# Kernel tuning notes

Measured on AMD Instinct MI355X. Metric: run time of the kernel, lower is better.

The kernel has to match this reference:

```python
import jax, jax.numpy as jnp
import numpy as np

NUM_HEADS = 16
HEAD_DIM = 64
WINDOW = 512
D_MODEL = NUM_HEADS * HEAD_DIM
BATCH = 2
SEQ = 2048


def setup_inputs() -> dict:
    key = jax.random.key(0)
    k1, k2, k3 = jax.random.split(key, 3)
    x = jax.random.normal(k1, (BATCH, SEQ, D_MODEL), dtype=jnp.float32)
    # Dense layer params (lecun_normal-like scale for stability)
    qkv_kernel = jax.random.normal(k2, (D_MODEL, 3 * NUM_HEADS * HEAD_DIM), dtype=jnp.float32) / np.sqrt(D_MODEL)
    qkv_bias = jnp.zeros((3 * NUM_HEADS * HEAD_DIM,), dtype=jnp.float32)
    out_kernel = jax.random.normal(k3, (NUM_HEADS * HEAD_DIM, D_MODEL), dtype=jnp.float32) / np.sqrt(D_MODEL)
    out_bias = jnp.zeros((D_MODEL,), dtype=jnp.float32)
    return {"x": x, "qkv_kernel": qkv_kernel, "qkv_bias": qkv_bias,
            "out_kernel": out_kernel, "out_bias": out_bias}


def reference(x, qkv_kernel, qkv_bias, out_kernel, out_bias):
    b, s, d = x.shape
    qkv = x @ qkv_kernel + qkv_bias                       # (b, s, 3*H*hd)
    qkv = qkv.reshape(b, s, 3, NUM_HEADS, HEAD_DIM)
    q = qkv[:, :, 0].transpose(0, 2, 1, 3)                # (b, H, s, hd)
    k = qkv[:, :, 1].transpose(0, 2, 1, 3)
    v = qkv[:, :, 2].transpose(0, 2, 1, 3)
    scale = 1.0 / jnp.sqrt(jnp.float32(HEAD_DIM)).astype(x.dtype)
    scores = jnp.einsum('bhqd,bhkd->bhqk', q, k) * scale  # (b, H, s, s)
    rows = jnp.arange(s)[:, None]
    cols = jnp.arange(s)[None, :]
    window_mask = (rows - cols >= 0) & (rows - cols < WINDOW)
    scores = jnp.where(window_mask[None, None], scores, jnp.asarray(-1e9, scores.dtype))
    attn = jax.nn.softmax(scores, axis=-1)
    out = jnp.einsum('bhqk,bhkd->bhqd', attn, v)          # (b, H, s, hd)
    out = out.transpose(0, 2, 1, 3).reshape(b, s, -1)
    return out @ out_kernel + out_bias
```

## Files before the change

### kernel.cpp

```cpp
#include <hip/hip_runtime.h>
#include <cstdint>
#include <cstddef>

#define NUM_HEADS 16
#define HEAD_DIM  64
#define WINDOW    512
#define D_MODEL   1024
#define BATCH     2
#define SEQ       2048
#define MTOT      (BATCH*SEQ)
#define NQKV      (3*D_MODEL)

typedef short bf16x8 __attribute__((ext_vector_type(8)));
typedef float f32x4  __attribute__((ext_vector_type(4)));

__device__ __forceinline__ f32x4 mfma16(bf16x8 a, bf16x8 b, f32x4 c) {
  return __builtin_amdgcn_mfma_f32_16x16x32_bf16(a, b, c, 0, 0, 0);
}

__device__ __forceinline__ unsigned short f2bf(float f) {
  unsigned int u = __float_as_uint(f);
  u += 0x7fffu + ((u >> 16) & 1u);
  return (unsigned short)(u >> 16);
}
__device__ __forceinline__ float bf2f(unsigned short b) {
  return __uint_as_float(((unsigned int)b) << 16);
}

__device__ __forceinline__ void gld16(const unsigned short* g, unsigned short* l) {
  __builtin_amdgcn_global_load_lds(
      (const __attribute__((address_space(1))) unsigned int*)g,
      (__attribute__((address_space(3))) unsigned int*)l, 16, 0, 0);
}

__global__ __launch_bounds__(256) void cvt_bf16_kernel(const float* __restrict__ in,
                                                       unsigned short* __restrict__ out) {
  int i = (blockIdx.x * 256 + threadIdx.x) * 4;
  float4 v = *(const float4*)(in + i);
  ushort4 o;
  o.x = f2bf(v.x); o.y = f2bf(v.y); o.z = f2bf(v.z); o.w = f2bf(v.w);
  *(ushort4*)(out + i) = o;
}

__global__ __launch_bounds__(256) void transpose_cvt_kernel(const float* __restrict__ in,
                                                            unsigned short* __restrict__ out,
                                                            int R, int C) {
  __shared__ float tile[32][33];
  int tx = threadIdx.x, ty = threadIdx.y;
  int c0 = blockIdx.x * 32, r0 = blockIdx.y * 32;
#pragma unroll
  for (int i = 0; i < 32; i += 8)
    tile[ty + i][tx] = in[(size_t)(r0 + ty + i) * C + c0 + tx];
  __syncthreads();
#pragma unroll
  for (int i = 0; i < 32; i += 8)
    out[(size_t)(c0 + ty + i) * R + r0 + tx] = f2bf(tile[tx][ty + i]);
}

template<bool SWAP>
__device__ __forceinline__ void gemm_mainloop(const unsigned short* __restrict__ A,
                                              const unsigned short* __restrict__ Bt,
                                              int K, int m0, int n0,
                                              unsigned short* sA, unsigned short* sB,
                                              f32x4 (&acc)[4][4]) {
  const int t = threadIdx.x;
  const int lane = t & 63, wave = t >> 6;
  const int wm = wave >> 1, wn = wave & 1;
  const int lhi = lane >> 4, llo = lane & 15;
  f32x4 zero = {0.f, 0.f, 0.f, 0.f};
#pragma unroll
  for (int i = 0; i < 4; ++i)
#pragma unroll
    for (int j = 0; j < 4; ++j) acc[i][j] = zero;

  const int cswz = (((t & 3) ^ ((t >> 3) & 3)) << 3);
  const unsigned short* gA = A  + (size_t)(m0 + (t >> 2)) * K + cswz;
  const unsigned short* gB = Bt + (size_t)(n0 + (t >> 2)) * K + cswz;
  const size_t rowskip = (size_t)64 * K;
  unsigned short* lA = sA + t * 8;
  unsigned short* lB = sB + t * 8;
  const int rsw = (lhi ^ ((llo >> 1) & 3)) * 8;
  const unsigned short* rA = sA + (wm * 64 + llo) * 32 + rsw;
  const unsigned short* rB = sB + (wn * 64 + llo) * 32 + rsw;

  for (int k0 = 0; k0 < K; k0 += 32) {
    gld16(gA, lA); gld16(gA + rowskip, lA + 2048);
    gld16(gB, lB); gld16(gB + rowskip, lB + 2048);
    gA += 32; gB += 32;
    __syncthreads();
    bf16x8 af[4], bfr[4];
#pragma unroll
    for (int i = 0; i < 4; ++i) af[i]  = *(const bf16x8*)(rA + i * 512);
#pragma unroll
    for (int i = 0; i < 4; ++i) bfr[i] = *(const bf16x8*)(rB + i * 512);
#pragma unroll
    for (int i = 0; i < 4; ++i)
#pragma unroll
      for (int j = 0; j < 4; ++j)
        acc[i][j] = SWAP ? mfma16(bfr[j], af[i], acc[i][j])
                         : mfma16(af[i], bfr[j], acc[i][j]);
    __syncthreads();
  }
}

__global__ __launch_bounds__(256) void qkv_gemm_kernel(const unsigned short* __restrict__ Xb,
                                                       const unsigned short* __restrict__ Wt,
                                                       const float* __restrict__ bias,
                                                       unsigned short* __restrict__ Qw,
                                                       unsigned short* __restrict__ Kw,
                                                       unsigned short* __restrict__ Vtw) {
  __shared__ __align__(16) unsigned short sA[128 * 32];
  __shared__ __align__(16) unsigned short sB[128 * 32];
  f32x4 acc[4][4];
  const int m0 = blockIdx.y * 128, n0 = blockIdx.x * 128;
  const int t = threadIdx.x, lane = t & 63, wave = t >> 6;
  const int wm = wave >> 1, wn = wave & 1, lhi = lane >> 4, llo = lane & 15;

  if (n0 < 2048) {
    gemm_mainloop<false>(Xb, Wt, D_MODEL, m0, n0, sA, sB, acc);
#pragma unroll
    for (int ti = 0; ti < 4; ++ti) {
#pragma unroll
      for (int tj = 0; tj < 4; ++tj) {
        int n = n0 + wn * 64 + tj * 16 + llo;
        float bv = bias[n];
        int c = n >> 10, h = (n >> 6) & 15, d = n & 63;
#pragma unroll
        for (int r = 0; r < 4; ++r) {
          int m = m0 + wm * 64 + ti * 16 + lhi * 4 + r;
          int b = m >> 11, s = m & 2047;
          int bh = b * 16 + h;
          float v = acc[ti][tj][r] + bv;
          size_t idx = ((size_t)(bh * 2048 + s)) * 64 + d;
          if (c == 0) Qw[idx] = f2bf(v * 0.125f);
          else        Kw[idx] = f2bf(v);
        }
      }
    }
  } else {
    gemm_mainloop<true>(Xb, Wt, D_MODEL, m0, n0, sA, sB, acc);
#pragma unroll
    for (int ti = 0; ti < 4; ++ti) {
      int m = m0 + wm * 64 + ti * 16 + llo;
      int b = m >> 11, s = m & 2047;
#pragma unroll
      for (int tj = 0; tj < 4; ++tj) {
        int nb = n0 + wn * 64 + tj * 16 + lhi * 4;
        float4 bv = *(const float4*)(bias + nb);
        int h = (nb >> 6) & 15, dbase = nb & 63;
        int bh = b * 16 + h;
        float bvr[4] = {bv.x, bv.y, bv.z, bv.w};
#pragma unroll
        for (int r = 0; r < 4; ++r)
          Vtw[(size_t)(bh * 64 + dbase + r) * 2048 + s] = f2bf(acc[ti][tj][r] + bvr[r]);
      }
    }
  }
}

__global__ __launch_bounds__(256) void attn_kernel(const unsigned short* __restrict__ Qw,
                                                   const unsigned short* __restrict__ Kw,
                                                   const unsigned short* __restrict__ Vtw,
                                                   unsigned short* __restrict__ AO) {
  __shared__ __align__(16) unsigned short sK[2][64 * 64];
  __shared__ __align__(16) unsigned short sV[2][64 * 64];
  __shared__ __align__(16) unsigned short sP[4][16 * 72];
  const int t = threadIdx.x, lane = t & 63, wave = t >> 6;
  const int lhi = lane >> 4, llo = lane & 15;
  const int bh = blockIdx.x;
  const int q0 = (15 - blockIdx.y) << 7;
  const unsigned short* Qb = Qw  + (size_t)bh * 2048 * 64;
  const unsigned short* Kb = Kw  + (size_t)bh * 2048 * 64;
  const unsigned short* Vb = Vtw + (size_t)bh * 64 * 2048;

  const int qrow0 = q0 + wave * 16 + llo;
  bf16x8 qf[2][2];
  qf[0][0] = *(const bf16x8*)(Qb + (size_t)qrow0 * 64 + lhi * 8);
  qf[0][1] = *(const bf16x8*)(Qb + (size_t)qrow0 * 64 + 32 + lhi * 8);
  qf[1][0] = *(const bf16x8*)(Qb + (size_t)(qrow0 + 64) * 64 + lhi * 8);
  qf[1][1] = *(const bf16x8*)(Qb + (size_t)(qrow0 + 64) * 64 + 32 + lhi * 8);

  const int srow = t >> 3;
  const int scol = ((t & 7) ^ (srow & 7)) * 8;
  const int cpos  = (lhi ^ (llo & 7)) * 8;
  const int cposx = cpos ^ 32;

  float m_i[2] = {-1e30f, -1e30f}, l_i[2] = {0.f, 0.f};
  f32x4 o[2][4];
  f32x4 zero = {0.f, 0.f, 0.f, 0.f};
#pragma unroll
  for (int qs = 0; qs < 2; ++qs)
#pragma unroll
    for (int td = 0; td < 4; ++td) o[qs][td] = zero;

  const int kt_lo = (q0 > 511) ? ((q0 - 511) >> 6) : 0;
  const int kt_hi = (q0 + 64) >> 6;

  {
    const int k0 = kt_lo << 6;
    unsigned short* dK = sK[kt_lo & 1];
    unsigned short* dV = sV[kt_lo & 1];
    gld16(Kb + (size_t)(k0 + srow) * 64 + scol,      dK + t * 8);
    gld16(Kb + (size_t)(k0 + srow + 32) * 64 + scol, dK + t * 8 + 2048);
    gld16(Vb + (size_t)srow * 2048 + k0 + scol,        dV + t * 8);
    gld16(Vb + (size_t)(srow + 32) * 2048 + k0 + scol, dV + t * 8 + 2048);
  }

  for (int kt = kt_lo; kt <= kt_hi; ++kt) {
    __syncthreads();
    if (kt < kt_hi) {
      const int k0n = (kt + 1) << 6;
      unsigned short* dK = sK[(kt + 1) & 1];
      unsigned short* dV = sV[(kt + 1) & 1];
      gld16(Kb + (size_t)(k0n + srow) * 64 + scol,      dK + t * 8);
      gld16(Kb + (size_t)(k0n + srow + 32) * 64 + scol, dK + t * 8 + 2048);
      gld16(Vb + (size_t)srow * 2048 + k0n + scol,        dV + t * 8);
      gld16(Vb + (size_t)(srow + 32) * 2048 + k0n + scol, dV + t * 8 + 2048);
    }
    const unsigned short* bK = sK[kt & 1];
    const unsigned short* bV = sV[kt & 1];
    const int k0 = kt << 6;

#pragma unroll
    for (int qs = 0; qs < 2; ++qs) {
      const int qmin = q0 + qs * 64;
      if (k0 > qmin + 63 || k0 + 63 < qmin - (WINDOW - 1)) continue;
      const int qrow = qrow0 + qs * 64;

      f32x4 st[4];
#pragma unroll
      for (int tk = 0; tk < 4; ++tk) {
        const unsigned short* kr = bK + (tk * 16 + llo) * 64;
        bf16x8 kf0 = *(const bf16x8*)(kr + cpos);
        bf16x8 kf1 = *(const bf16x8*)(kr + cposx);
        f32x4 z = zero;
        z = mfma16(kf0, qf[qs][0], z);
        z = mfma16(kf1, qf[qs][1], z);
        st[tk] = z;
      }

      const int kb = k0 + lhi * 4;
      float mx = -1e30f;
#pragma unroll
      for (int tk = 0; tk < 4; ++tk)
#pragma unroll
        for (int r = 0; r < 4; ++r) {
          int key = kb + tk * 16 + r;
          bool ok = (key <= qrow) && (qrow - key < WINDOW);
          float s = ok ? st[tk][r] : -1e30f;
          st[tk][r] = s;
          mx = fmaxf(mx, s);
        }
      mx = fmaxf(mx, __shfl_xor(mx, 16));
      mx = fmaxf(mx, __shfl_xor(mx, 32));
      float mn = fmaxf(m_i[qs], mx);
      float a  = __expf(m_i[qs] - mn);
      float rs = 0.f;
      unsigned short* pw = &sP[wave][llo * 72];
#pragma unroll
      for (int tk = 0; tk < 4; ++tk) {
        ushort4 pb;
        pb.x = f2bf(__expf(st[tk][0] - mn));
        pb.y = f2bf(__expf(st[tk][1] - mn));
        pb.z = f2bf(__expf(st[tk][2] - mn));
        pb.w = f2bf(__expf(st[tk][3] - mn));
        *(ushort4*)(pw + tk * 16 + lhi * 4) = pb;
        rs += bf2f(pb.x) + bf2f(pb.y) + bf2f(pb.z) + bf2f(pb.w);
      }
      rs += __shfl_xor(rs, 16);
      rs += __shfl_xor(rs, 32);
      l_i[qs] = l_i[qs] * a + rs;
      m_i[qs] = mn;

      float aR[4];
#pragma unroll
      for (int r = 0; r < 4; ++r) aR[r] = __shfl(a, lhi * 4 + r);
#pragma unroll
      for (int td = 0; td < 4; ++td)
#pragma unroll
        for (int r = 0; r < 4; ++r) o[qs][td][r] *= aR[r];

      bf16x8 pf0 = *(const bf16x8*)(pw + lhi * 8);
      bf16x8 pf1 = *(const bf16x8*)(pw + 32 + lhi * 8);
#pragma unroll
      for (int td = 0; td < 4; ++td) {
        const unsigned short* vr = bV + (td * 16 + llo) * 64;
        bf16x8 vf0 = *(const bf16x8*)(vr + cpos);
        bf16x8 vf1 = *(const bf16x8*)(vr + cposx);
        o[qs][td] = mfma16(pf0, vf0, o[qs][td]);
        o[qs][td] = mfma16(pf1, vf1, o[qs][td]);
      }
    }
  }

  const int b = bh >> 4, h = bh & 15;
#pragma unroll
  for (int qs = 0; qs < 2; ++qs) {
    float lR[4];
#pragma unroll
    for (int r = 0; r < 4; ++r) lR[r] = 1.f / __shfl(l_i[qs], lhi * 4 + r);
#pragma unroll
    for (int td = 0; td < 4; ++td)
#pragma unroll
      for (int r = 0; r < 4; ++r) {
        int qr = q0 + qs * 64 + wave * 16 + lhi * 4 + r;
        AO[(size_t)(b * 2048 + qr) * 1024 + h * 64 + td * 16 + llo] = f2bf(o[qs][td][r] * lR[r]);
      }
  }
}

__global__ __launch_bounds__(256) void out_gemm_kernel(const unsigned short* __restrict__ AO,
                                                       const unsigned short* __restrict__ Wt,
                                                       const float* __restrict__ bias,
                                                       float* __restrict__ out) {
  __shared__ __align__(16) unsigned short sA[128 * 32];
  __shared__ __align__(16) unsigned short sB[128 * 32];
  f32x4 acc[4][4];
  const int m0 = blockIdx.y * 128, n0 = blockIdx.x * 128;
  gemm_mainloop<false>(AO, Wt, D_MODEL, m0, n0, sA, sB, acc);

  const int t = threadIdx.x, lane = t & 63, wave = t >> 6;
  const int wm = wave >> 1, wn = wave & 1, lhi = lane >> 4, llo = lane & 15;
#pragma unroll
  for (int ti = 0; ti < 4; ++ti)
#pragma unroll
    for (int tj = 0; tj < 4; ++tj) {
      int n = n0 + wn * 64 + tj * 16 + llo;
      float bv = bias[n];
#pragma unroll
      for (int r = 0; r < 4; ++r) {
        int m = m0 + wm * 64 + ti * 16 + lhi * 4 + r;
        out[(size_t)m * D_MODEL + n] = acc[ti][tj][r] + bv;
      }
    }
}

extern "C" void kernel_launch(void* const* d_in, const int* in_sizes, int n_in,
                              void* d_out, int out_size, void* d_ws, size_t ws_size,
                              hipStream_t stream) {
  const float* x      = (const float*)d_in[0];
  const float* qkv_w  = (const float*)d_in[1];
  const float* qkv_b  = (const float*)d_in[2];
  const float* out_w  = (const float*)d_in[3];
  const float* out_b  = (const float*)d_in[4];
  float* out = (float*)d_out;
  char* ws = (char*)d_ws;

  unsigned short* Xb  = (unsigned short*)(ws);
  unsigned short* Wq  = (unsigned short*)(ws + ((size_t)8  << 20));
  unsigned short* Wo  = (unsigned short*)(ws + ((size_t)14 << 20));
  unsigned short* Qw  = (unsigned short*)(ws + ((size_t)16 << 20));
  unsigned short* Kw  = (unsigned short*)(ws + ((size_t)24 << 20));
  unsigned short* Vtw = (unsigned short*)(ws + ((size_t)32 << 20));
  unsigned short* AO  = (unsigned short*)(ws + ((size_t)40 << 20));

  cvt_bf16_kernel<<<MTOT * D_MODEL / 1024, 256, 0, stream>>>(x, Xb);
  transpose_cvt_kernel<<<dim3(NQKV / 32, D_MODEL / 32), dim3(32, 8), 0, stream>>>(qkv_w, Wq, D_MODEL, NQKV);
  transpose_cvt_kernel<<<dim3(D_MODEL / 32, D_MODEL / 32), dim3(32, 8), 0, stream>>>(out_w, Wo, D_MODEL, D_MODEL);
  qkv_gemm_kernel<<<dim3(NQKV / 128, MTOT / 128), 256, 0, stream>>>(Xb, Wq, qkv_b, Qw, Kw, Vtw);
  attn_kernel<<<dim3(BATCH * NUM_HEADS, SEQ / 128), 256, 0, stream>>>(Qw, Kw, Vtw, AO);
  out_gemm_kernel<<<dim3(D_MODEL / 128, MTOT / 128), 256, 0, stream>>>(AO, Wo, out_b, out);
}
```

Before: 190.7 us.

## Fuse prep kernels, double-buffer GEMM LDS, shrink attention and out-GEMM tiles

Merges the input conversion and both weight transposes into one prep launch. Double-buffers the GEMM shared-memory tiles so the next K slice loads while the current one computes, and drops one barrier per iteration. Attention blocks now cover 64 query rows instead of 128, and the output GEMM uses 64-row tiles; both double the block count for better occupancy at the cost of reloading more K/V and weight tiles. Doubling the LDS footprint may lower the number of resident blocks per CU.

```diff
diff --git a/kernel.cpp b/kernel.cpp
--- a/kernel.cpp
+++ b/kernel.cpp
@@ -33,21 +33,27 @@
       (__attribute__((address_space(3))) unsigned int*)l, 16, 0, 0);
 }
 
-__global__ __launch_bounds__(256) void cvt_bf16_kernel(const float* __restrict__ in,
-                                                       unsigned short* __restrict__ out) {
-  int i = (blockIdx.x * 256 + threadIdx.x) * 4;
-  float4 v = *(const float4*)(in + i);
-  ushort4 o;
-  o.x = f2bf(v.x); o.y = f2bf(v.y); o.z = f2bf(v.z); o.w = f2bf(v.w);
-  *(ushort4*)(out + i) = o;
-}
-
-__global__ __launch_bounds__(256) void transpose_cvt_kernel(const float* __restrict__ in,
-                                                            unsigned short* __restrict__ out,
-                                                            int R, int C) {
+__global__ __launch_bounds__(256) void prep_kernel(const float* __restrict__ x,
+                                                   const float* __restrict__ qkv_w,
+                                                   const float* __restrict__ out_w,
+                                                   unsigned short* __restrict__ Xb,
+                                                   unsigned short* __restrict__ Wq,
+                                                   unsigned short* __restrict__ Wo) {
   __shared__ float tile[32][33];
-  int tx = threadIdx.x, ty = threadIdx.y;
-  int c0 = blockIdx.x * 32, r0 = blockIdx.y * 32;
+  const int bid = blockIdx.x, t = threadIdx.x;
+  if (bid < 4096) {
+    int i = (bid * 256 + t) * 4;
+    float4 v = *(const float4*)(x + i);
+    ushort4 o;
+    o.x = f2bf(v.x); o.y = f2bf(v.y); o.z = f2bf(v.z); o.w = f2bf(v.w);
+    *(ushort4*)(Xb + i) = o;
+    return;
+  }
+  const float* in; unsigned short* out; int R, C, bx, by;
+  if (bid < 7168) { int b2 = bid - 4096; in = qkv_w; out = Wq; R = D_MODEL; C = NQKV; bx = b2 % 96; by = b2 / 96; }
+  else            { int b2 = bid - 7168; in = out_w; out = Wo; R = D_MODEL; C = D_MODEL; bx = b2 & 31; by = b2 >> 5; }
+  int tx = t & 31, ty = t >> 5;
+  int c0 = bx * 32, r0 = by * 32;
 #pragma unroll
   for (int i = 0; i < 32; i += 8)
     tile[ty + i][tx] = in[(size_t)(r0 + ty + i) * C + c0 + tx];
@@ -57,19 +63,20 @@
     out[(size_t)(c0 + ty + i) * R + r0 + tx] = f2bf(tile[tx][ty + i]);
 }
 
-template<bool SWAP>
-__device__ __forceinline__ void gemm_mainloop(const unsigned short* __restrict__ A,
-                                              const unsigned short* __restrict__ Bt,
-                                              int K, int m0, int n0,
-                                              unsigned short* sA, unsigned short* sB,
-                                              f32x4 (&acc)[4][4]) {
+template<int TI, bool SWAP>
+__device__ __forceinline__ void gemm_mainloop_db(const unsigned short* __restrict__ A,
+                                                 const unsigned short* __restrict__ Bt,
+                                                 int K, int m0, int n0,
+                                                 unsigned short* sA0, unsigned short* sA1,
+                                                 unsigned short* sB0, unsigned short* sB1,
+                                                 f32x4 (&acc)[TI][4]) {
   const int t = threadIdx.x;
   const int lane = t & 63, wave = t >> 6;
   const int wm = wave >> 1, wn = wave & 1;
   const int lhi = lane >> 4, llo = lane & 15;
   f32x4 zero = {0.f, 0.f, 0.f, 0.f};
 #pragma unroll
-  for (int i = 0; i < 4; ++i)
+  for (int i = 0; i < TI; ++i)
 #pragma unroll
     for (int j = 0; j < 4; ++j) acc[i][j] = zero;
 
@@ -77,29 +84,41 @@
   const unsigned short* gA = A  + (size_t)(m0 + (t >> 2)) * K + cswz;
   const unsigned short* gB = Bt + (size_t)(n0 + (t >> 2)) * K + cswz;
   const size_t rowskip = (size_t)64 * K;
-  unsigned short* lA = sA + t * 8;
-  unsigned short* lB = sB + t * 8;
-  const int rsw = (lhi ^ ((llo >> 1) & 3)) * 8;
-  const unsigned short* rA = sA + (wm * 64 + llo) * 32 + rsw;
-  const unsigned short* rB = sB + (wn * 64 + llo) * 32 + rsw;
-
-  for (int k0 = 0; k0 < K; k0 += 32) {
-    gld16(gA, lA); gld16(gA + rowskip, lA + 2048);
-    gld16(gB, lB); gld16(gB + rowskip, lB + 2048);
-    gA += 32; gB += 32;
+  const int ldsT = t * 8;
+  const int rsw  = (lhi ^ ((llo >> 1) & 3)) * 8;
+  const int aoff = (wm * (TI * 16) + llo) * 32 + rsw;
+  const int boff = (wn * 64 + llo) * 32 + rsw;
+
+  gld16(gA, sA0 + ldsT);
+  if (TI == 4) gld16(gA + rowskip, sA0 + ldsT + 2048);
+  gld16(gB, sB0 + ldsT);
+  gld16(gB + rowskip, sB0 + ldsT + 2048);
+
+  const int nIter = K >> 5;
+  for (int it = 0; it < nIter; ++it) {
     __syncthreads();
-    bf16x8 af[4], bfr[4];
-#pragma unroll
-    for (int i = 0; i < 4; ++i) af[i]  = *(const bf16x8*)(rA + i * 512);
-#pragma unroll
-    for (int i = 0; i < 4; ++i) bfr[i] = *(const bf16x8*)(rB + i * 512);
-#pragma unroll
-    for (int i = 0; i < 4; ++i)
+    unsigned short* cA = (it & 1) ? sA1 : sA0;
+    unsigned short* cB = (it & 1) ? sB1 : sB0;
+    if (it + 1 < nIter) {
+      unsigned short* nA = (it & 1) ? sA0 : sA1;
+      unsigned short* nB = (it & 1) ? sB0 : sB1;
+      gA += 32; gB += 32;
+      gld16(gA, nA + ldsT);
+      if (TI == 4) gld16(gA + rowskip, nA + ldsT + 2048);
+      gld16(gB, nB + ldsT);
+      gld16(gB + rowskip, nB + ldsT + 2048);
+    }
+    bf16x8 af[TI], bfr[4];
+#pragma unroll
+    for (int i = 0; i < TI; ++i) af[i]  = *(const bf16x8*)(cA + aoff + i * 512);
+#pragma unroll
+    for (int j = 0; j < 4; ++j)  bfr[j] = *(const bf16x8*)(cB + boff + j * 512);
+#pragma unroll
+    for (int i = 0; i < TI; ++i)
 #pragma unroll
       for (int j = 0; j < 4; ++j)
         acc[i][j] = SWAP ? mfma16(bfr[j], af[i], acc[i][j])
                          : mfma16(af[i], bfr[j], acc[i][j]);
-    __syncthreads();
   }
 }
 
@@ -109,15 +128,15 @@
                                                        unsigned short* __restrict__ Qw,
                                                        unsigned short* __restrict__ Kw,
                                                        unsigned short* __restrict__ Vtw) {
-  __shared__ __align__(16) unsigned short sA[128 * 32];
-  __shared__ __align__(16) unsigned short sB[128 * 32];
+  __shared__ __align__(16) unsigned short sA[2][128 * 32];
+  __shared__ __align__(16) unsigned short sB[2][128 * 32];
   f32x4 acc[4][4];
   const int m0 = blockIdx.y * 128, n0 = blockIdx.x * 128;
   const int t = threadIdx.x, lane = t & 63, wave = t >> 6;
   const int wm = wave >> 1, wn = wave & 1, lhi = lane >> 4, llo = lane & 15;
 
   if (n0 < 2048) {
-    gemm_mainloop<false>(Xb, Wt, D_MODEL, m0, n0, sA, sB, acc);
+    gemm_mainloop_db<4, false>(Xb, Wt, D_MODEL, m0, n0, sA[0], sA[1], sB[0], sB[1], acc);
 #pragma unroll
     for (int ti = 0; ti < 4; ++ti) {
 #pragma unroll
@@ -138,7 +157,7 @@
       }
     }
   } else {
-    gemm_mainloop<true>(Xb, Wt, D_MODEL, m0, n0, sA, sB, acc);
+    gemm_mainloop_db<4, true>(Xb, Wt, D_MODEL, m0, n0, sA[0], sA[1], sB[0], sB[1], acc);
 #pragma unroll
     for (int ti = 0; ti < 4; ++ti) {
       int m = m0 + wm * 64 + ti * 16 + llo;
@@ -168,33 +187,28 @@
   const int t = threadIdx.x, lane = t & 63, wave = t >> 6;
   const int lhi = lane >> 4, llo = lane & 15;
   const int bh = blockIdx.x;
-  const int q0 = (15 - blockIdx.y) << 7;
+  const int q0 = (31 - blockIdx.y) << 6;
   const unsigned short* Qb = Qw  + (size_t)bh * 2048 * 64;
   const unsigned short* Kb = Kw  + (size_t)bh * 2048 * 64;
   const unsigned short* Vb = Vtw + (size_t)bh * 64 * 2048;
 
-  const int qrow0 = q0 + wave * 16 + llo;
-  bf16x8 qf[2][2];
-  qf[0][0] = *(const bf16x8*)(Qb + (size_t)qrow0 * 64 + lhi * 8);
-  qf[0][1] = *(const bf16x8*)(Qb + (size_t)qrow0 * 64 + 32 + lhi * 8);
-  qf[1][0] = *(const bf16x8*)(Qb + (size_t)(qrow0 + 64) * 64 + lhi * 8);
-  qf[1][1] = *(const bf16x8*)(Qb + (size_t)(qrow0 + 64) * 64 + 32 + lhi * 8);
+  const int qrow = q0 + wave * 16 + llo;
+  bf16x8 qf0 = *(const bf16x8*)(Qb + (size_t)qrow * 64 + lhi * 8);
+  bf16x8 qf1 = *(const bf16x8*)(Qb + (size_t)qrow * 64 + 32 + lhi * 8);
 
   const int srow = t >> 3;
   const int scol = ((t & 7) ^ (srow & 7)) * 8;
   const int cpos  = (lhi ^ (llo & 7)) * 8;
   const int cposx = cpos ^ 32;
 
-  float m_i[2] = {-1e30f, -1e30f}, l_i[2] = {0.f, 0.f};
-  f32x4 o[2][4];
+  float m_i = -1e30f, l_i = 0.f;
+  f32x4 o[4];
   f32x4 zero = {0.f, 0.f, 0.f, 0.f};
 #pragma unroll
-  for (int qs = 0; qs < 2; ++qs)
-#pragma unroll
-    for (int td = 0; td < 4; ++td) o[qs][td] = zero;
+  for (int td = 0; td < 4; ++td) o[td] = zero;
 
   const int kt_lo = (q0 > 511) ? ((q0 - 511) >> 6) : 0;
-  const int kt_hi = (q0 + 64) >> 6;
+  const int kt_hi = q0 >> 6;
 
   {
     const int k0 = kt_lo << 6;
@@ -221,115 +235,105 @@
     const unsigned short* bV = sV[kt & 1];
     const int k0 = kt << 6;
 
-#pragma unroll
-    for (int qs = 0; qs < 2; ++qs) {
-      const int qmin = q0 + qs * 64;
-      if (k0 > qmin + 63 || k0 + 63 < qmin - (WINDOW - 1)) continue;
-      const int qrow = qrow0 + qs * 64;
-
-      f32x4 st[4];
-#pragma unroll
-      for (int tk = 0; tk < 4; ++tk) {
-        const unsigned short* kr = bK + (tk * 16 + llo) * 64;
-        bf16x8 kf0 = *(const bf16x8*)(kr + cpos);
-        bf16x8 kf1 = *(const bf16x8*)(kr + cposx);
-        f32x4 z = zero;
-        z = mfma16(kf0, qf[qs][0], z);
-        z = mfma16(kf1, qf[qs][1], z);
-        st[tk] = z;
+    f32x4 st[4];
+#pragma unroll
+    for (int tk = 0; tk < 4; ++tk) {
+      const unsigned short* kr = bK + (tk * 16 + llo) * 64;
+      bf16x8 kf0 = *(const bf16x8*)(kr + cpos);
+      bf16x8 kf1 = *(const bf16x8*)(kr + cposx);
+      f32x4 z = zero;
+      z = mfma16(kf0, qf0, z);
+      z = mfma16(kf1, qf1, z);
+      st[tk] = z;
+    }
+
+    const int kb = k0 + lhi * 4;
+    float mx = -1e30f;
+#pragma unroll
+    for (int tk = 0; tk < 4; ++tk)
+#pragma unroll
+      for (int r = 0; r < 4; ++r) {
+        int key = kb + tk * 16 + r;
+        bool ok = (key <= qrow) && (qrow - key < WINDOW);
+        float s = ok ? st[tk][r] : -1e30f;
+        st[tk][r] = s;
+        mx = fmaxf(mx, s);
       }
-
-      const int kb = k0 + lhi * 4;
-      float mx = -1e30f;
-#pragma unroll
-      for (int tk = 0; tk < 4; ++tk)
-#pragma unroll
-        for (int r = 0; r < 4; ++r) {
-          int key = kb + tk * 16 + r;
-          bool ok = (key <= qrow) && (qrow - key < WINDOW);
-          float s = ok ? st[tk][r] : -1e30f;
-          st[tk][r] = s;
-          mx = fmaxf(mx, s);
-        }
-      mx = fmaxf(mx, __shfl_xor(mx, 16));
-      mx = fmaxf(mx, __shfl_xor(mx, 32));
-      float mn = fmaxf(m_i[qs], mx);
-      float a  = __expf(m_i[qs] - mn);
-      float rs = 0.f;
-      unsigned short* pw = &sP[wave][llo * 72];
-#pragma unroll
-      for (int tk = 0; tk < 4; ++tk) {
-        ushort4 pb;
-        pb.x = f2bf(__expf(st[tk][0] - mn));
-        pb.y = f2bf(__expf(st[tk][1] - mn));
-        pb.z = f2bf(__expf(st[tk][2] - mn));
-        pb.w = f2bf(__expf(st[tk][3] - mn));
-        *(ushort4*)(pw + tk * 16 + lhi * 4) = pb;
-        rs += bf2f(pb.x) + bf2f(pb.y) + bf2f(pb.z) + bf2f(pb.w);
-      }
-      rs += __shfl_xor(rs, 16);
-      rs += __shfl_xor(rs, 32);
-      l_i[qs] = l_i[qs] * a + rs;
-      m_i[qs] = mn;
-
-      float aR[4];
-#pragma unroll
-      for (int r = 0; r < 4; ++r) aR[r] = __shfl(a, lhi * 4 + r);
-#pragma unroll
-      for (int td = 0; td < 4; ++td)
-#pragma unroll
-        for (int r = 0; r < 4; ++r) o[qs][td][r] *= aR[r];
-
-      bf16x8 pf0 = *(const bf16x8*)(pw + lhi * 8);
-      bf16x8 pf1 = *(const bf16x8*)(pw + 32 + lhi * 8);
-#pragma unroll
-      for (int td = 0; td < 4; ++td) {
-        const unsigned short* vr = bV + (td * 16 + llo) * 64;
-        bf16x8 vf0 = *(const bf16x8*)(vr + cpos);
-        bf16x8 vf1 = *(const bf16x8*)(vr + cposx);
-        o[qs][td] = mfma16(pf0, vf0, o[qs][td]);
-        o[qs][td] = mfma16(pf1, vf1, o[qs][td]);
-      }
-    }
-  }
-
+    mx = fmaxf(mx, __shfl_xor(mx, 16));
+    mx = fmaxf(mx, __shfl_xor(mx, 32));
+    float mn = fmaxf(m_i, mx);
+    float a  = __expf(m_i - mn);
+    float rs = 0.f;
+    unsigned short* pw = &sP[wave][llo * 72];
+#pragma unroll
+    for (int tk = 0; tk < 4; ++tk) {
+      ushort4 pb;
+      pb.x = f2bf(__expf(st[tk][0] - mn));
+      pb.y = f2bf(__expf(st[tk][1] - mn));
+      pb.z = f2bf(__expf(st[tk][2] - mn));
+      pb.w = f2bf(__expf(st[tk][3] - mn));
+      *(ushort4*)(pw + tk * 16 + lhi * 4) = pb;
+      rs += bf2f(pb.x) + bf2f(pb.y) + bf2f(pb.z) + bf2f(pb.w);
+    }
+    rs += __shfl_xor(rs, 16);
+    rs += __shfl_xor(rs, 32);
+    l_i = l_i * a + rs;
+    m_i = mn;
+
+    float aR[4];
+#pragma unroll
+    for (int r = 0; r < 4; ++r) aR[r] = __shfl(a, lhi * 4 + r);
+#pragma unroll
+    for (int td = 0; td < 4; ++td)
+#pragma unroll
+      for (int r = 0; r < 4; ++r) o[td][r] *= aR[r];
+
+    bf16x8 pf0 = *(const bf16x8*)(pw + lhi * 8);
+    bf16x8 pf1 = *(const bf16x8*)(pw + 32 + lhi * 8);
+#pragma unroll
+    for (int td = 0; td < 4; ++td) {
+      const unsigned short* vr = bV + (td * 16 + llo) * 64;
+      bf16x8 vf0 = *(const bf16x8*)(vr + cpos);
+      bf16x8 vf1 = *(const bf16x8*)(vr + cposx);
+      o[td] = mfma16(pf0, vf0, o[td]);
+      o[td] = mfma16(pf1, vf1, o[td]);
+    }
+  }
+
+  float lR[4];
+#pragma unroll
+  for (int r = 0; r < 4; ++r) lR[r] = 1.f / __shfl(l_i, lhi * 4 + r);
   const int b = bh >> 4, h = bh & 15;
 #pragma unroll
-  for (int qs = 0; qs < 2; ++qs) {
-    float lR[4];
-#pragma unroll
-    for (int r = 0; r < 4; ++r) lR[r] = 1.f / __shfl(l_i[qs], lhi * 4 + r);
-#pragma unroll
-    for (int td = 0; td < 4; ++td)
-#pragma unroll
-      for (int r = 0; r < 4; ++r) {
-        int qr = q0 + qs * 64 + wave * 16 + lhi * 4 + r;
-        AO[(size_t)(b * 2048 + qr) * 1024 + h * 64 + td * 16 + llo] = f2bf(o[qs][td][r] * lR[r]);
-      }
-  }
+  for (int td = 0; td < 4; ++td)
+#pragma unroll
+    for (int r = 0; r < 4; ++r) {
+      int qr = q0 + wave * 16 + lhi * 4 + r;
+      AO[(size_t)(b * 2048 + qr) * 1024 + h * 64 + td * 16 + llo] = f2bf(o[td][r] * lR[r]);
+    }
 }
 
 __global__ __launch_bounds__(256) void out_gemm_kernel(const unsigned short* __restrict__ AO,
                                                        const unsigned short* __restrict__ Wt,
                                                        const float* __restrict__ bias,
                                                        float* __restrict__ out) {
-  __shared__ __align__(16) unsigned short sA[128 * 32];
-  __shared__ __align__(16) unsigned short sB[128 * 32];
-  f32x4 acc[4][4];
-  const int m0 = blockIdx.y * 128, n0 = blockIdx.x * 128;
-  gemm_mainloop<false>(AO, Wt, D_MODEL, m0, n0, sA, sB, acc);
+  __shared__ __align__(16) unsigned short sA[2][64 * 32];
+  __shared__ __align__(16) unsigned short sB[2][128 * 32];
+  f32x4 acc[2][4];
+  const int m0 = blockIdx.y * 64, n0 = blockIdx.x * 128;
+  gemm_mainloop_db<2, false>(AO, Wt, D_MODEL, m0, n0, sA[0], sA[1], sB[0], sB[1], acc);
 
   const int t = threadIdx.x, lane = t & 63, wave = t >> 6;
   const int wm = wave >> 1, wn = wave & 1, lhi = lane >> 4, llo = lane & 15;
 #pragma unroll
-  for (int ti = 0; ti < 4; ++ti)
+  for (int ti = 0; ti < 2; ++ti)
 #pragma unroll
     for (int tj = 0; tj < 4; ++tj) {
       int n = n0 + wn * 64 + tj * 16 + llo;
       float bv = bias[n];
 #pragma unroll
       for (int r = 0; r < 4; ++r) {
-        int m = m0 + wm * 64 + ti * 16 + lhi * 4 + r;
+        int m = m0 + wm * 32 + ti * 16 + lhi * 4 + r;
         out[(size_t)m * D_MODEL + n] = acc[ti][tj][r] + bv;
       }
     }
@@ -354,10 +358,8 @@
   unsigned short* Vtw = (unsigned short*)(ws + ((size_t)32 << 20));
   unsigned short* AO  = (unsigned short*)(ws + ((size_t)40 << 20));
 
-  cvt_bf16_kernel<<<MTOT * D_MODEL / 1024, 256, 0, stream>>>(x, Xb);
-  transpose_cvt_kernel<<<dim3(NQKV / 32, D_MODEL / 32), dim3(32, 8), 0, stream>>>(qkv_w, Wq, D_MODEL, NQKV);
-  transpose_cvt_kernel<<<dim3(D_MODEL / 32, D_MODEL / 32), dim3(32, 8), 0, stream>>>(out_w, Wo, D_MODEL, D_MODEL);
+  prep_kernel<<<8192, 256, 0, stream>>>(x, qkv_w, out_w, Xb, Wq, Wo);
   qkv_gemm_kernel<<<dim3(NQKV / 128, MTOT / 128), 256, 0, stream>>>(Xb, Wq, qkv_b, Qw, Kw, Vtw);
-  attn_kernel<<<dim3(BATCH * NUM_HEADS, SEQ / 128), 256, 0, stream>>>(Qw, Kw, Vtw, AO);
-  out_gemm_kernel<<<dim3(D_MODEL / 128, MTOT / 128), 256, 0, stream>>>(AO, Wo, out_b, out);
-}
+  attn_kernel<<<dim3(BATCH * NUM_HEADS, SEQ / 64), 256, 0, stream>>>(Qw, Kw, Vtw, AO);
+  out_gemm_kernel<<<dim3(D_MODEL / 128, MTOT / 64), 256, 0, stream>>>(AO, Wo, out_b, out);
+}
```

Result: faster. 172.5 us (-9.5%).
